# Performance work log

Measured on AMD Instinct MI355X. Metric: run time of the kernel, lower is better.

Reference implementation:

```python
import jax, jax.numpy as jnp
import numpy as np

D_MODEL = 1024
N_HEADS = 16
HEAD_DIM = D_MODEL // N_HEADS  # 64
TOP_K = 64
EPS = 1e-12  # matches F.normalize eps


def setup_inputs() -> dict:
    key = jax.random.key(0)
    ks = jax.random.split(key, 6)
    s = 0.02
    def w(k):
        return jax.random.normal(k, (D_MODEL, D_MODEL), jnp.float32) * s
    zb = jnp.zeros((D_MODEL,), jnp.float32)
    # x: (B, T, d_model); T must equal d_model (see compress_proj constraint)
    x = jax.random.normal(ks[0], (2, 1024, D_MODEL), jnp.float32)
    return {
        "x": x,
        "Wq": w(ks[1]), "bq": zb,
        "Wk": w(ks[2]), "bk": zb,
        "Wv": w(ks[3]), "bv": zb,
        "Wo": w(ks[4]), "bo": zb,
        "Wc": w(ks[5]), "bc": zb,  # compress_proj (applied along time axis)
    }


def _l2norm(a):
    n = jnp.linalg.norm(a, axis=-1, keepdims=True)
    return a / jnp.maximum(n, EPS)


def reference(x, Wq, bq, Wk, bk, Wv, bv, Wo, bo, Wc, bc):
    B, T, Dm = x.shape
    H, hd = N_HEADS, HEAD_DIM

    def proj(W, b):
        return (x @ W.T + b).reshape(B, T, H, hd).transpose(0, 2, 1, 3)  # (B,H,T,hd)

    Q = proj(Wq, bq)
    K = proj(Wk, bk)
    V = proj(Wv, bv)

    # compress_kv with compress_ratio=1: compress_proj acts on the (transposed)
    # time axis, so K_comp[b,h,c,d] = sum_t K[b,h,t,d] * Wc[c,t] + bc[c]
    K_comp = jnp.einsum('bhtd,ct->bhcd', K, Wc) + bc[None, None, :, None]
    V_comp = jnp.einsum('bhtd,ct->bhcd', V, Wc) + bc[None, None, :, None]

    # lightning indexer: cosine similarity + top-k over compressed slots
    sim = jnp.einsum('bhtd,bhcd->bhtc', _l2norm(Q), _l2norm(K_comp))
    topk_idx = jax.lax.top_k(sim, TOP_K)[1]  # (B,H,T,K)

    bi = jnp.arange(B)[:, None, None, None]
    hi = jnp.arange(H)[None, :, None, None]
    K_sel = K_comp[bi, hi, topk_idx]  # (B,H,T,K,hd)
    V_sel = V_comp[bi, hi, topk_idx]

    scores = jnp.einsum('bhtd,bhtkd->bhtk', Q, K_sel) / float(np.sqrt(hd))
    attn = jax.nn.softmax(scores, axis=-1)
    out = jnp.einsum('bhtk,bhtkd->bhtd', attn, V_sel)  # (B,H,T,hd)
    out = out.transpose(0, 2, 1, 3).reshape(B, T, Dm)
    return out @ Wo.T + bo
```

## Files before the change

### kernel.cpp

```cpp
#include <hip/hip_runtime.h>
#include <type_traits>


#define DEVI __device__ __forceinline__

constexpr int Tn = 1024;
constexpr int Cn = 1024;
constexpr int Hn = 16;

typedef short bf16x8 __attribute__((ext_vector_type(8)));
typedef float f32x4 __attribute__((ext_vector_type(4)));
typedef double f64x4 __attribute__((ext_vector_type(4)));

DEVI int wsumi(int v)   { for (int m = 1; m < 64; m <<= 1) v += __shfl_xor(v, m); return v; }
DEVI int wmini(int v)   { for (int m = 1; m < 64; m <<= 1) { int o = __shfl_xor(v, m); v = o < v ? o : v; } return v; }
DEVI float wfmax(float v){ for (int m = 1; m < 64; m <<= 1) v = fmaxf(v, __shfl_xor(v, m)); return v; }
DEVI float wfsum(float v){ for (int m = 1; m < 64; m <<= 1) v += __shfl_xor(v, m); return v; }

DEVI unsigned long long mapd(double x) {
  unsigned long long b = (unsigned long long)__double_as_longlong(x);
  return (b >> 63) ? ~b : (b | 0x8000000000000000ull);
}

DEVI unsigned short f2bf_rne(float x) {
  unsigned u = __float_as_uint(x);
  u += 0x7fffu + ((u >> 16) & 1u);
  return (unsigned short)(u >> 16);
}
struct BfPair { short hi, lo; };
DEVI BfPair split2(float x) {
  unsigned short h = f2bf_rne(x);
  float hf = __uint_as_float(((unsigned)h) << 16);
  BfPair r;
  r.hi = (short)h;
  r.lo = (short)f2bf_rne(x - hf);
  return r;
}

template <typename OUTT, bool BTRANS, int BIASMODE, bool SIM>
__global__ __launch_bounds__(256) void f64sel_k(
    const float* __restrict__ A, const float* __restrict__ B,
    const float* __restrict__ bias, OUTT* __restrict__ C,
    int Kd, int lda, int ldb, int ldc,
    long long zB, long long zC, int group_base)
{
  __shared__ float As[16][72];
  __shared__ float Bs[16][72];

  size_t offA = 0, offB = 0, offC = 0;
  if (SIM) {
    int pair = group_base + (int)blockIdx.z;
    int bb = pair >> 4, hh = pair & 15;
    offA = ((size_t)bb * Tn) * (size_t)lda + (size_t)hh * 64;
    offB = ((size_t)bb * Cn) * (size_t)ldb + (size_t)hh * 64;
    offC = (size_t)blockIdx.z * (size_t)Tn * (size_t)ldc;
  } else {
    offB = (size_t)blockIdx.z * (size_t)zB;
    offC = (size_t)blockIdx.z * (size_t)zC;
  }
  const float* Ab = A + offA;
  const float* Bb = B + offB;
  OUTT* Cb = C + offC;

  const int tid = threadIdx.x;
  const int lane = tid & 63, w = tid >> 6;
  const int wr = w >> 1, wc = w & 1;
  const int l15 = lane & 15, l4 = lane >> 4;
  const int m0 = blockIdx.y * 64, n0 = blockIdx.x * 64;

  f64x4 zz = {0.0, 0.0, 0.0, 0.0};
  f64x4 p1 = __builtin_amdgcn_mfma_f64_16x16x4f64(1.0, (double)l15, zz, 0, 0, 0);
  f64x4 p2 = __builtin_amdgcn_mfma_f64_16x16x4f64((double)l15, 1.0, zz, 0, 0, 0);
  int a1 = 1, b1 = 1, c1 = 1, a2 = 1, b2 = 1, c2 = 1;
#pragma unroll
  for (int rr = 0; rr < 4; ++rr) {
    a1 &= (p1[rr] == 4.0 * l15);
    b1 &= (p1[rr] == 4.0 * (l4 * 4 + rr));
    c1 &= (p1[rr] == 4.0 * (l4 + 4 * rr));
    a2 &= (p2[rr] == 4.0 * (l4 * 4 + rr));
    b2 &= (p2[rr] == 4.0 * (l4 + 4 * rr));
    c2 &= (p2[rr] == 4.0 * l15);
  }
  a1 = __all(a1); b1 = __all(b1); c1 = __all(c1);
  a2 = __all(a2); b2 = __all(b2); c2 = __all(c2);
  int dmap = 0, useM = 1;
  if      (a1 && a2) dmap = 0;
  else if (a1 && b2) dmap = 1;
  else if (b1 && c2) dmap = 2;
  else if (c1 && c2) dmap = 3;
  else useM = 0;

  f64x4 acc[2][2];
#pragma unroll
  for (int i = 0; i < 2; ++i)
#pragma unroll
    for (int j = 0; j < 2; ++j) acc[i][j] = (f64x4){0.0, 0.0, 0.0, 0.0};

  for (int k0 = 0; k0 < Kd; k0 += 16) {
    {
      int m = tid >> 2, kf = tid & 3;
      float4 a = *(const float4*)(Ab + (size_t)(m0 + m) * lda + k0 + 4 * kf);
      As[4 * kf + 0][m] = a.x; As[4 * kf + 1][m] = a.y;
      As[4 * kf + 2][m] = a.z; As[4 * kf + 3][m] = a.w;
    }
    if (BTRANS) {
      int n = tid >> 2, kf = tid & 3;
      float4 b = *(const float4*)(Bb + (size_t)(n0 + n) * ldb + k0 + 4 * kf);
      Bs[4 * kf + 0][n] = b.x; Bs[4 * kf + 1][n] = b.y;
      Bs[4 * kf + 2][n] = b.z; Bs[4 * kf + 3][n] = b.w;
    } else {
      int k = tid >> 4, nf = tid & 15;
      float4 b = *(const float4*)(Bb + (size_t)(k0 + k) * ldb + n0 + 4 * nf);
      *(float4*)&Bs[k][4 * nf] = b;
    }
    __syncthreads();

    if (useM) {
#pragma unroll
      for (int kq = 0; kq < 4; ++kq) {
        int kk = kq * 4 + l4;
        double a0  = (double)As[kk][wr * 32 + l15];
        double a1v = (double)As[kk][wr * 32 + 16 + l15];
        double b0  = (double)Bs[kk][wc * 32 + l15];
        double b1v = (double)Bs[kk][wc * 32 + 16 + l15];
        acc[0][0] = __builtin_amdgcn_mfma_f64_16x16x4f64(a0,  b0,  acc[0][0], 0, 0, 0);
        acc[0][1] = __builtin_amdgcn_mfma_f64_16x16x4f64(a0,  b1v, acc[0][1], 0, 0, 0);
        acc[1][0] = __builtin_amdgcn_mfma_f64_16x16x4f64(a1v, b0,  acc[1][0], 0, 0, 0);
        acc[1][1] = __builtin_amdgcn_mfma_f64_16x16x4f64(a1v, b1v, acc[1][1], 0, 0, 0);
      }
    } else {
#pragma unroll
      for (int k = 0; k < 16; ++k) {
        double bv0 = (double)Bs[k][wc * 32 + l15];
        double bv1 = (double)Bs[k][wc * 32 + 16 + l15];
#pragma unroll
        for (int fr = 0; fr < 2; ++fr)
#pragma unroll
          for (int rr = 0; rr < 4; ++rr) {
            double av = (double)As[k][wr * 32 + fr * 16 + l4 * 4 + rr];
            acc[fr][0][rr] += av * bv0;
            acc[fr][1][rr] += av * bv1;
          }
      }
    }
    __syncthreads();
  }

#pragma unroll
  for (int fr = 0; fr < 2; ++fr)
#pragma unroll
    for (int fc = 0; fc < 2; ++fc)
#pragma unroll
      for (int rr = 0; rr < 4; ++rr) {
        int ri, ci;
        if (!useM || dmap == 0) { ri = l4 * 4 + rr; ci = l15; }
        else if (dmap == 1)     { ri = l4 + 4 * rr; ci = l15; }
        else if (dmap == 2)     { ri = l15; ci = l4 * 4 + rr; }
        else                    { ri = l15; ci = l4 + 4 * rr; }
        int row = m0 + wr * 32 + fr * 16 + ri;
        int col = n0 + wc * 32 + fc * 16 + ci;
        double v = acc[fr][fc][rr];
        if constexpr (std::is_same<OUTT, double>::value) {
          Cb[(size_t)row * ldc + col] = v;
        } else {
          float s = (float)v;
          float cb = (BIASMODE == 1) ? bias[col] : 0.f;
          float rb = (BIASMODE == 2) ? bias[row] : 0.f;
          ((float*)Cb)[(size_t)row * ldc + col] = s + cb + rb;
        }
      }
}

template <bool BTRANS, int BIASMODE>
__global__ __launch_bounds__(256) void mfma_gemm_k(
    const float* __restrict__ A, const float* __restrict__ B,
    const float* __restrict__ bias, float* __restrict__ C,
    int Kd, int lda, int ldb, int ldc, long long zB, long long zC)
{
  __shared__ short Ah[4 * 64 * 8];
  __shared__ short Al[4 * 64 * 8];
  __shared__ short Bh[4 * 64 * 8];
  __shared__ short Bl[4 * 64 * 8];

  const float* Bz = B + (size_t)blockIdx.z * (size_t)zB;
  float* Cz = C + (size_t)blockIdx.z * (size_t)zC;

  const int tid = threadIdx.x;
  const int lane = tid & 63, w = tid >> 6;
  const int wr = w >> 1, wc = w & 1;
  const int m0 = blockIdx.y * 64, n0 = blockIdx.x * 64;
  const int r16 = lane & 15, kg = lane >> 4;

  f32x4 acc[2][2];
#pragma unroll
  for (int i = 0; i < 2; ++i)
#pragma unroll
    for (int j = 0; j < 2; ++j) acc[i][j] = (f32x4){0.f, 0.f, 0.f, 0.f};

  for (int k0 = 0; k0 < Kd; k0 += 32) {
    {
      int row = tid >> 2, kseg = tid & 3;
      const float* p = A + (size_t)(m0 + row) * lda + k0 + kseg * 8;
      float4 v0 = *(const float4*)p;
      float4 v1 = *(const float4*)(p + 4);
      BfPair q0 = split2(v0.x), q1 = split2(v0.y), q2 = split2(v0.z), q3 = split2(v0.w);
      BfPair q4 = split2(v1.x), q5 = split2(v1.y), q6 = split2(v1.z), q7 = split2(v1.w);
      bf16x8 h = {q0.hi, q1.hi, q2.hi, q3.hi, q4.hi, q5.hi, q6.hi, q7.hi};
      bf16x8 l = {q0.lo, q1.lo, q2.lo, q3.lo, q4.lo, q5.lo, q6.lo, q7.lo};
      int idx = (kseg * 64 + row) * 8;
      *(bf16x8*)&Ah[idx] = h;
      *(bf16x8*)&Al[idx] = l;
    }
    if (BTRANS) {
      int row = tid >> 2, kseg = tid & 3;
      const float* p = Bz + (size_t)(n0 + row) * ldb + k0 + kseg * 8;
      float4 v0 = *(const float4*)p;
      float4 v1 = *(const float4*)(p + 4);
      BfPair q0 = split2(v0.x), q1 = split2(v0.y), q2 = split2(v0.z), q3 = split2(v0.w);
      BfPair q4 = split2(v1.x), q5 = split2(v1.y), q6 = split2(v1.z), q7 = split2(v1.w);
      bf16x8 h = {q0.hi, q1.hi, q2.hi, q3.hi, q4.hi, q5.hi, q6.hi, q7.hi};
      bf16x8 l = {q0.lo, q1.lo, q2.lo, q3.lo, q4.lo, q5.lo, q6.lo, q7.lo};
      int idx = (kseg * 64 + row) * 8;
      *(bf16x8*)&Bh[idx] = h;
      *(bf16x8*)&Bl[idx] = l;
    } else {
      int col = tid & 63, kseg = tid >> 6;
      short hv[8], lv[8];
#pragma unroll
      for (int j = 0; j < 8; ++j) {
        BfPair p = split2(Bz[(size_t)(k0 + kseg * 8 + j) * ldb + n0 + col]);
        hv[j] = p.hi; lv[j] = p.lo;
      }
      bf16x8 h = {hv[0], hv[1], hv[2], hv[3], hv[4], hv[5], hv[6], hv[7]};
      bf16x8 l = {lv[0], lv[1], lv[2], lv[3], lv[4], lv[5], lv[6], lv[7]};
      int idx = (kseg * 64 + col) * 8;
      *(bf16x8*)&Bh[idx] = h;
      *(bf16x8*)&Bl[idx] = l;
    }
    __syncthreads();

    bf16x8 ah[2], al[2], bh[2], bl[2];
#pragma unroll
    for (int f = 0; f < 2; ++f) {
      int ia = (kg * 64 + wr * 32 + f * 16 + r16) * 8;
      int ib = (kg * 64 + wc * 32 + f * 16 + r16) * 8;
      ah[f] = *(const bf16x8*)&Ah[ia];
      al[f] = *(const bf16x8*)&Al[ia];
      bh[f] = *(const bf16x8*)&Bh[ib];
      bl[f] = *(const bf16x8*)&Bl[ib];
    }
#pragma unroll
    for (int fr = 0; fr < 2; ++fr)
#pragma unroll
      for (int fc = 0; fc < 2; ++fc) {
        f32x4 c = acc[fr][fc];
        c = __builtin_amdgcn_mfma_f32_16x16x32_bf16(al[fr], bh[fc], c, 0, 0, 0);
        c = __builtin_amdgcn_mfma_f32_16x16x32_bf16(ah[fr], bl[fc], c, 0, 0, 0);
        c = __builtin_amdgcn_mfma_f32_16x16x32_bf16(ah[fr], bh[fc], c, 0, 0, 0);
        acc[fr][fc] = c;
      }
    __syncthreads();
  }

#pragma unroll
  for (int fr = 0; fr < 2; ++fr)
#pragma unroll
    for (int fc = 0; fc < 2; ++fc) {
      int col = n0 + wc * 32 + fc * 16 + r16;
      float cb = (BIASMODE == 1) ? bias[col] : 0.f;
#pragma unroll
      for (int rr = 0; rr < 4; ++rr) {
        int rw = m0 + wr * 32 + fr * 16 + kg * 4 + rr;
        float rb = (BIASMODE == 2) ? bias[rw] : 0.f;
        Cz[(size_t)rw * ldc + col] = acc[fr][fc][rr] + cb + rb;
      }
    }
}

__global__ __launch_bounds__(256) void kn_k2(const float* __restrict__ Kc,
                                             double* __restrict__ kn)
{
  int idx = (int)blockIdx.x * 256 + (int)threadIdx.x;
  int c = idx & 1023;
  int p = idx >> 10;
  int b = p >> 4, h = p & 15;
  const float* row = Kc + ((size_t)(b * 1024 + c)) * 1024 + h * 64;
  double s = 0.0;
  for (int d = 0; d < 64; ++d) { double v = (double)row[d]; s += v * v; }
  kn[(size_t)p * 1024 + c] = 1.0 / fmax(sqrt(s), 1e-12);
}

__global__ __launch_bounds__(256) void topk_attn_k(
    const double* __restrict__ dotb, const double* __restrict__ kn,
    const float* __restrict__ Vc, float* __restrict__ attnout, int group_base)
{
  __shared__ int sC[4][64];
  __shared__ float sD[4][64];

  const int lane = threadIdx.x & 63, wv = threadIdx.x >> 6;
  const int g = (int)blockIdx.x >> 8;
  const int t = ((int)blockIdx.x & 255) * 4 + wv;
  const int pair = group_base + g;
  const int bb = pair >> 4, hh = pair & 15;

  const double* drow = dotb + ((size_t)g * Tn + t) * (size_t)Cn;
  const double* knr  = kn + ((size_t)(bb * Hn + hh)) * Cn;

  double dv[16];
  unsigned long long u[16];
#pragma unroll
  for (int j = 0; j < 8; ++j) {
    double2 dd = *(const double2*)(drow + j * 128 + 2 * lane);
    double2 kk = *(const double2*)(knr  + j * 128 + 2 * lane);
    dv[2 * j] = dd.x; dv[2 * j + 1] = dd.y;
    u[2 * j]     = mapd(dd.x * kk.x);
    u[2 * j + 1] = mapd(dd.y * kk.y);
  }
  unsigned hi[16];
#pragma unroll
  for (int i = 0; i < 16; ++i) hi[i] = (unsigned)(u[i] >> 32);

  unsigned TH = 0;
  for (int bit = 31; bit >= 0; --bit) {
    unsigned Tc = TH | (1u << bit);
    int c = 0;
#pragma unroll
    for (int i = 0; i < 16; ++i) c += (hi[i] >= Tc);
    if (wsumi(c) >= 64) TH = Tc;
  }
  int mhi = 0;
#pragma unroll
  for (int i = 0; i < 16; ++i) mhi += (hi[i] > TH);
  mhi = wsumi(mhi);
  const int need1 = 64 - mhi;
  unsigned TL = 0;
  for (int bit = 31; bit >= 0; --bit) {
    unsigned Tc = TL | (1u << bit);
    int c = 0;
#pragma unroll
    for (int i = 0; i < 16; ++i) c += (hi[i] == TH && (unsigned)u[i] >= Tc);
    if (wsumi(c) >= need1) TL = Tc;
  }
  const unsigned long long V64 = ((unsigned long long)TH << 32) | TL;

  int base = 0;
#pragma unroll
  for (int i = 0; i < 16; ++i) {
    const int cix = 128 * (i >> 1) + 2 * lane + (i & 1);
    bool sel = (u[i] > V64);
    unsigned long long mk = __ballot(sel);
    if (sel) {
      int r = __popcll(mk & ((1ull << lane) - 1ull));
      sC[wv][base + r] = cix;
      sD[wv][base + r] = (float)dv[i];
    }
    base += __popcll(mk);
  }
  const int need = 64 - base;
  unsigned taken = 0;
  for (int r = 0; r < need; ++r) {
    int mn = 0x7fffffff;
#pragma unroll
    for (int i = 0; i < 16; ++i) {
      int cix = 128 * (i >> 1) + 2 * lane + (i & 1);
      if (u[i] == V64 && !((taken >> i) & 1u)) mn = mn < cix ? mn : cix;
    }
    mn = wmini(mn);
#pragma unroll
    for (int i = 0; i < 16; ++i) {
      int cix = 128 * (i >> 1) + 2 * lane + (i & 1);
      if (u[i] == V64 && !((taken >> i) & 1u) && cix == mn) {
        taken |= 1u << i;
        sC[wv][base + r] = mn;
        sD[wv][base + r] = (float)dv[i];
      }
    }
  }
  __syncthreads();

  int ck = sC[wv][lane];
  float sc = sD[wv][lane] * 0.125f;
  float mx = wfmax(sc);
  float w = expf(sc - mx);
  float sw = wfsum(w);
  w /= sw;

  const float* Vb = Vc + (size_t)bb * ((size_t)Cn * 1024) + hh * 64 + lane;
  float acc = 0.f;
#pragma unroll 4
  for (int k = 0; k < 64; ++k) {
    int c = __shfl(ck, k);
    float wk = __shfl(w, k);
    acc = fmaf(wk, Vb[(size_t)c * 1024], acc);
  }
  attnout[((size_t)(bb * Tn + t)) * 1024 + hh * 64 + lane] = acc;
}

extern "C" void kernel_launch(void* const* d_in, const int* in_sizes, int n_in,
                              void* d_out, int out_size, void* d_ws, size_t ws_size,
                              hipStream_t stream)
{
  const float* x  = (const float*)d_in[0];
  const float* Wq = (const float*)d_in[1];
  const float* bq = (const float*)d_in[2];
  const float* Wk = (const float*)d_in[3];
  const float* bk = (const float*)d_in[4];
  const float* Wv = (const float*)d_in[5];
  const float* bv = (const float*)d_in[6];
  const float* Wo = (const float*)d_in[7];
  const float* bo = (const float*)d_in[8];
  const float* Wc = (const float*)d_in[9];
  const float* bc = (const float*)d_in[10];
  float* out = (float*)d_out;

  const size_t NE = (size_t)2048 * 1024;
  const size_t M1 = (size_t)1024 * 1024;
  float* Q   = (float*)d_ws;
  float* Kf  = Q + NE;
  float* Vf  = Kf + NE;
  float* Kc  = Vf + NE;
  float* Vc  = Kc + NE;
  float* at  = Vc + NE;
  double* kn = (double*)(at + NE);
  double* tail = kn + 32768;

  const size_t fixedB = 6 * NE * 4 + 32768 * 8;
  const size_t dotPairB = (size_t)Tn * Cn * 8;
  if (ws_size < fixedB) return;

  size_t rem = ws_size - fixedB;
  double* dotp; int G;
  if      (rem >= 8 * dotPairB) { G = 8; dotp = tail; }
  else if (rem >= 4 * dotPairB) { G = 4; dotp = tail; }
  else if (rem >= 2 * dotPairB) { G = 2; dotp = tail; }
  else { G = 2; dotp = (double*)Kf; }

  dim3 blk(256, 1, 1);

  f64sel_k<float, true, 1, false><<<dim3(16, 32, 1), blk, 0, stream>>>(
      x, Wq, bq, Q, 1024, 1024, 1024, 1024, 0, 0, 0);
  f64sel_k<float, true, 1, false><<<dim3(16, 32, 1), blk, 0, stream>>>(
      x, Wk, bk, Kf, 1024, 1024, 1024, 1024, 0, 0, 0);
  mfma_gemm_k<true, 1><<<dim3(16, 32, 1), blk, 0, stream>>>(
      x, Wv, bv, Vf, 1024, 1024, 1024, 1024, 0, 0);

  f64sel_k<float, false, 2, false><<<dim3(16, 16, 2), blk, 0, stream>>>(
      Wc, Kf, bc, Kc, 1024, 1024, 1024, 1024, (long long)M1, (long long)M1, 0);
  mfma_gemm_k<false, 2><<<dim3(16, 16, 2), blk, 0, stream>>>(
      Wc, Vf, bc, Vc, 1024, 1024, 1024, 1024, (long long)M1, (long long)M1);

  kn_k2<<<dim3(128), blk, 0, stream>>>(Kc, kn);

  for (int gb = 0; gb < 32; gb += G) {
    f64sel_k<double, true, 0, true><<<dim3(16, 16, G), blk, 0, stream>>>(
        Q, Kc, nullptr, dotp, 64, 1024, 1024, 1024, 0, 0, gb);
    topk_attn_k<<<dim3(256 * G), blk, 0, stream>>>(dotp, kn, Vc, at, gb);
  }

  mfma_gemm_k<true, 1><<<dim3(16, 32, 1), blk, 0, stream>>>(
      at, Wo, bo, out, 1024, 1024, 1024, 1024, 0, 0);
}
```

Measured before the change: 889.4 us.

## Register-prefetch next K tile in both GEMM kernels and widen f64 tile to 32

Both GEMM kernels now load the next K-slice from global memory into registers after the barrier, so the loads overlap with the MFMA work on the current shared-memory tile. The f64 kernel also doubles its K tile from 16 to 32, which halves the number of barrier rounds per output tile. In exchange it uses more registers and shared memory, which may reduce occupancy. It also assumes Kd is a multiple of 32.

```diff
diff --git a/kernel.cpp b/kernel.cpp
--- a/kernel.cpp
+++ b/kernel.cpp
@@ -44,8 +44,8 @@
     int Kd, int lda, int ldb, int ldc,
     long long zB, long long zC, int group_base)
 {
-  __shared__ float As[16][72];
-  __shared__ float Bs[16][72];
+  __shared__ float As[32][72];
+  __shared__ float Bs[32][72];
 
   size_t offA = 0, offB = 0, offC = 0;
   if (SIM) {
@@ -96,28 +96,55 @@
 #pragma unroll
     for (int j = 0; j < 2; ++j) acc[i][j] = (f64x4){0.0, 0.0, 0.0, 0.0};
 
-  for (int k0 = 0; k0 < Kd; k0 += 16) {
-    {
-      int m = tid >> 2, kf = tid & 3;
-      float4 a = *(const float4*)(Ab + (size_t)(m0 + m) * lda + k0 + 4 * kf);
-      As[4 * kf + 0][m] = a.x; As[4 * kf + 1][m] = a.y;
-      As[4 * kf + 2][m] = a.z; As[4 * kf + 3][m] = a.w;
-    }
+  const int sm = tid >> 2, skf = tid & 3;
+  const int bkl = tid >> 4, bnf = tid & 15;
+
+  const int nT = Kd >> 5;
+  float4 a0_, a1_, b0_, b1_;
+  {
+    a0_ = *(const float4*)(Ab + (size_t)(m0 + sm) * lda + 4 * skf);
+    a1_ = *(const float4*)(Ab + (size_t)(m0 + sm) * lda + 16 + 4 * skf);
     if (BTRANS) {
-      int n = tid >> 2, kf = tid & 3;
-      float4 b = *(const float4*)(Bb + (size_t)(n0 + n) * ldb + k0 + 4 * kf);
-      Bs[4 * kf + 0][n] = b.x; Bs[4 * kf + 1][n] = b.y;
-      Bs[4 * kf + 2][n] = b.z; Bs[4 * kf + 3][n] = b.w;
+      b0_ = *(const float4*)(Bb + (size_t)(n0 + sm) * ldb + 4 * skf);
+      b1_ = *(const float4*)(Bb + (size_t)(n0 + sm) * ldb + 16 + 4 * skf);
     } else {
-      int k = tid >> 4, nf = tid & 15;
-      float4 b = *(const float4*)(Bb + (size_t)(k0 + k) * ldb + n0 + 4 * nf);
-      *(float4*)&Bs[k][4 * nf] = b;
+      b0_ = *(const float4*)(Bb + (size_t)bkl * ldb + n0 + 4 * bnf);
+      b1_ = *(const float4*)(Bb + (size_t)(16 + bkl) * ldb + n0 + 4 * bnf);
+    }
+  }
+
+  for (int kt = 0; kt < nT; ++kt) {
+    As[4 * skf + 0][sm] = a0_.x; As[4 * skf + 1][sm] = a0_.y;
+    As[4 * skf + 2][sm] = a0_.z; As[4 * skf + 3][sm] = a0_.w;
+    As[16 + 4 * skf + 0][sm] = a1_.x; As[16 + 4 * skf + 1][sm] = a1_.y;
+    As[16 + 4 * skf + 2][sm] = a1_.z; As[16 + 4 * skf + 3][sm] = a1_.w;
+    if (BTRANS) {
+      Bs[4 * skf + 0][sm] = b0_.x; Bs[4 * skf + 1][sm] = b0_.y;
+      Bs[4 * skf + 2][sm] = b0_.z; Bs[4 * skf + 3][sm] = b0_.w;
+      Bs[16 + 4 * skf + 0][sm] = b1_.x; Bs[16 + 4 * skf + 1][sm] = b1_.y;
+      Bs[16 + 4 * skf + 2][sm] = b1_.z; Bs[16 + 4 * skf + 3][sm] = b1_.w;
+    } else {
+      *(float4*)&Bs[bkl][4 * bnf] = b0_;
+      *(float4*)&Bs[16 + bkl][4 * bnf] = b1_;
     }
     __syncthreads();
 
+    if (kt + 1 < nT) {
+      int k0 = (kt + 1) * 32;
+      a0_ = *(const float4*)(Ab + (size_t)(m0 + sm) * lda + k0 + 4 * skf);
+      a1_ = *(const float4*)(Ab + (size_t)(m0 + sm) * lda + k0 + 16 + 4 * skf);
+      if (BTRANS) {
+        b0_ = *(const float4*)(Bb + (size_t)(n0 + sm) * ldb + k0 + 4 * skf);
+        b1_ = *(const float4*)(Bb + (size_t)(n0 + sm) * ldb + k0 + 16 + 4 * skf);
+      } else {
+        b0_ = *(const float4*)(Bb + (size_t)(k0 + bkl) * ldb + n0 + 4 * bnf);
+        b1_ = *(const float4*)(Bb + (size_t)(k0 + 16 + bkl) * ldb + n0 + 4 * bnf);
+      }
+    }
+
     if (useM) {
 #pragma unroll
-      for (int kq = 0; kq < 4; ++kq) {
+      for (int kq = 0; kq < 8; ++kq) {
         int kk = kq * 4 + l4;
         double a0  = (double)As[kk][wr * 32 + l15];
         double a1v = (double)As[kk][wr * 32 + 16 + l15];
@@ -130,7 +157,7 @@
       }
     } else {
 #pragma unroll
-      for (int k = 0; k < 16; ++k) {
+      for (int k = 0; k < 32; ++k) {
         double bv0 = (double)Bs[k][wc * 32 + l15];
         double bv1 = (double)Bs[k][wc * 32 + 16 + l15];
 #pragma unroll
@@ -197,14 +224,29 @@
 #pragma unroll
     for (int j = 0; j < 2; ++j) acc[i][j] = (f32x4){0.f, 0.f, 0.f, 0.f};
 
-  for (int k0 = 0; k0 < Kd; k0 += 32) {
+  const int row = tid >> 2, kseg = tid & 3;
+  const int gcol = tid & 63, gks = tid >> 6;
+
+  const int nT = Kd >> 5;
+  float4 pa0, pa1, pb0, pb1;
+  float gb[8];
+  {
+    pa0 = *(const float4*)(A + (size_t)(m0 + row) * lda + kseg * 8);
+    pa1 = *(const float4*)(A + (size_t)(m0 + row) * lda + kseg * 8 + 4);
+    if (BTRANS) {
+      pb0 = *(const float4*)(Bz + (size_t)(n0 + row) * ldb + kseg * 8);
+      pb1 = *(const float4*)(Bz + (size_t)(n0 + row) * ldb + kseg * 8 + 4);
+    } else {
+#pragma unroll
+      for (int j = 0; j < 8; ++j)
+        gb[j] = Bz[(size_t)(gks * 8 + j) * ldb + n0 + gcol];
+    }
+  }
+
+  for (int kt = 0; kt < nT; ++kt) {
     {
-      int row = tid >> 2, kseg = tid & 3;
-      const float* p = A + (size_t)(m0 + row) * lda + k0 + kseg * 8;
-      float4 v0 = *(const float4*)p;
-      float4 v1 = *(const float4*)(p + 4);
-      BfPair q0 = split2(v0.x), q1 = split2(v0.y), q2 = split2(v0.z), q3 = split2(v0.w);
-      BfPair q4 = split2(v1.x), q5 = split2(v1.y), q6 = split2(v1.z), q7 = split2(v1.w);
+      BfPair q0 = split2(pa0.x), q1 = split2(pa0.y), q2 = split2(pa0.z), q3 = split2(pa0.w);
+      BfPair q4 = split2(pa1.x), q5 = split2(pa1.y), q6 = split2(pa1.z), q7 = split2(pa1.w);
       bf16x8 h = {q0.hi, q1.hi, q2.hi, q3.hi, q4.hi, q5.hi, q6.hi, q7.hi};
       bf16x8 l = {q0.lo, q1.lo, q2.lo, q3.lo, q4.lo, q5.lo, q6.lo, q7.lo};
       int idx = (kseg * 64 + row) * 8;
@@ -212,32 +254,41 @@
       *(bf16x8*)&Al[idx] = l;
     }
     if (BTRANS) {
-      int row = tid >> 2, kseg = tid & 3;
-      const float* p = Bz + (size_t)(n0 + row) * ldb + k0 + kseg * 8;
-      float4 v0 = *(const float4*)p;
-      float4 v1 = *(const float4*)(p + 4);
-      BfPair q0 = split2(v0.x), q1 = split2(v0.y), q2 = split2(v0.z), q3 = split2(v0.w);
-      BfPair q4 = split2(v1.x), q5 = split2(v1.y), q6 = split2(v1.z), q7 = split2(v1.w);
+      BfPair q0 = split2(pb0.x), q1 = split2(pb0.y), q2 = split2(pb0.z), q3 = split2(pb0.w);
+      BfPair q4 = split2(pb1.x), q5 = split2(pb1.y), q6 = split2(pb1.z), q7 = split2(pb1.w);
       bf16x8 h = {q0.hi, q1.hi, q2.hi, q3.hi, q4.hi, q5.hi, q6.hi, q7.hi};
       bf16x8 l = {q0.lo, q1.lo, q2.lo, q3.lo, q4.lo, q5.lo, q6.lo, q7.lo};
       int idx = (kseg * 64 + row) * 8;
       *(bf16x8*)&Bh[idx] = h;
       *(bf16x8*)&Bl[idx] = l;
     } else {
-      int col = tid & 63, kseg = tid >> 6;
       short hv[8], lv[8];
 #pragma unroll
       for (int j = 0; j < 8; ++j) {
-        BfPair p = split2(Bz[(size_t)(k0 + kseg * 8 + j) * ldb + n0 + col]);
+        BfPair p = split2(gb[j]);
         hv[j] = p.hi; lv[j] = p.lo;
       }
       bf16x8 h = {hv[0], hv[1], hv[2], hv[3], hv[4], hv[5], hv[6], hv[7]};
       bf16x8 l = {lv[0], lv[1], lv[2], lv[3], lv[4], lv[5], lv[6], lv[7]};
-      int idx = (kseg * 64 + col) * 8;
+      int idx = (gks * 64 + gcol) * 8;
       *(bf16x8*)&Bh[idx] = h;
       *(bf16x8*)&Bl[idx] = l;
     }
     __syncthreads();
+
+    if (kt + 1 < nT) {
+      int k0 = (kt + 1) * 32;
+      pa0 = *(const float4*)(A + (size_t)(m0 + row) * lda + k0 + kseg * 8);
+      pa1 = *(const float4*)(A + (size_t)(m0 + row) * lda + k0 + kseg * 8 + 4);
+      if (BTRANS) {
+        pb0 = *(const float4*)(Bz + (size_t)(n0 + row) * ldb + k0 + kseg * 8);
+        pb1 = *(const float4*)(Bz + (size_t)(n0 + row) * ldb + k0 + kseg * 8 + 4);
+      } else {
+#pragma unroll
+        for (int j = 0; j < 8; ++j)
+          gb[j] = Bz[(size_t)(k0 + gks * 8 + j) * ldb + n0 + gcol];
+      }
+    }
 
     bf16x8 ah[2], al[2], bh[2], bl[2];
 #pragma unroll
```

Measured after the change: 856.8 us. -3.7%, faster.
